# Performance work log

Measured on AMD Instinct MI355X. Metric: run time of the kernel, lower is better.

Reference implementation:

```python
import jax, jax.numpy as jnp
import numpy as np

B, N, K, DIM, NB, RES, PAD = 2, 8192, 16, 64, 5, 64, 0.1
H = DIM // 2  # bottleneck width of FKABlock
PLANES = ((0, 1), (0, 2), (1, 2))  # xy, xz, yz


def setup_inputs() -> dict:
    key = jax.random.key(0)
    ks = jax.random.split(key, 10)
    xyz = jax.random.uniform(ks[0], (B, N, 3), jnp.float32) - 0.5

    def w(k, shape, fan_in):
        return jax.random.normal(k, shape, jnp.float32) / np.sqrt(fan_in)

    return {
        "xyz": xyz,
        "w_stem": w(ks[1], (3, DIM), 3),
        "b_stem": jnp.zeros((DIM,), jnp.float32),
        "w0": w(ks[2], (NB, DIM, H), DIM),
        "b0": jnp.zeros((NB, H), jnp.float32),
        "fc1": w(ks[3], (NB, 3, K), 3),
        "fc2": w(ks[4], (NB, 2 * K, K), 2 * K),
        "fc3": w(ks[5], (NB, 2 * K, K), 2 * K),
        "wcv": w(ks[6], (NB, H, H, K), H * K),
        "alpha": jnp.ones((NB,), jnp.float32),
        "beta": jnp.ones((NB,), jnp.float32),
        "w2": w(ks[7], (NB, H, DIM), H),
        "b2": jnp.zeros((NB, DIM), jnp.float32),
    }


def _knn_idx(xyz, k):
    # brute-force squared distances (b, n, n); top-k smallest -> neighbor indices
    sq = jnp.sum(xyz * xyz, -1)
    d2 = sq[:, :, None] + sq[:, None, :] - 2.0 * jnp.einsum('bnd,bmd->bnm', xyz, xyz)
    _, idx = jax.lax.top_k(-d2, k)
    return idx  # (b, n, k) int32


_gather = jax.vmap(lambda f, i: f[i])  # (n, c), (n, k) -> (n, k, c), vmapped over batch


def _fkaconv(x, xyz, idx, fc1, fc2, fc3, wcv, alpha, beta):
    nb_pos = _gather(xyz, idx)                 # (b, n, k, 3)
    pts = nb_pos - xyz[:, :, None, :]          # local coordinates
    # distances are detached in the original (pts.detach())
    dists = jnp.sqrt(jnp.sum(jax.lax.stop_gradient(pts) ** 2, -1) + 1e-12)  # (b, n, k)
    dw = jax.nn.sigmoid(-alpha * dists + beta)
    dw = dw / (jnp.sum(dw, -1, keepdims=True) + 1e-6) * K
    dwe = dw[..., None]                        # (b, n, k, 1)
    # kernel-weight estimation MLP with masked max-pool over neighbors
    m = jax.nn.relu(pts @ fc1)                 # (b, n, k, K)
    mp = jnp.max(m * dwe, 2, keepdims=True)
    m = jax.nn.relu(jnp.concatenate([m, jnp.broadcast_to(mp, m.shape)], -1) @ fc2)
    mp = jnp.max(m * dwe, 2, keepdims=True)
    m = jax.nn.relu(jnp.concatenate([m, jnp.broadcast_to(mp, m.shape)], -1) @ fc3)
    m = m * dwe                                # (b, n, k, K)
    nb_x = _gather(x, idx)                     # (b, n, k, h)
    # f[b,n,c,s] = sum_k nb_x * m ; out[b,n,o] = sum_{c,s} f * wcv[o,c,s]
    return jnp.einsum('bnkc,bnks,ocs->bno', nb_x, m, wcv)


def _triplane(c, xyz):
    pn = xyz / (1.0 + PAD + 1e-3) + 0.5        # normalize to [0, 1]
    ij = jnp.clip((pn * RES).astype(jnp.int32), 0, RES - 1)  # (b, n, 3)
    bidx = jnp.arange(B, dtype=jnp.int32)[:, None]
    cf = c.reshape(B * N, DIM)
    ones = jnp.ones((B * N,), c.dtype)
    planes = []
    for a, b2 in PLANES:
        seg = (bidx * (RES * RES) + ij[..., a] * RES + ij[..., b2]).reshape(-1)
        s = jax.ops.segment_sum(cf, seg, num_segments=B * RES * RES)
        cnt = jax.ops.segment_sum(ones, seg, num_segments=B * RES * RES)
        planes.append((s / jnp.maximum(cnt, 1.0)[:, None]).reshape(B, RES, RES, DIM))
    return jnp.stack(planes, 1)                # (b, 3, res, res, dim)


def reference(xyz, w_stem, b_stem, w0, b0, fc1, fc2, fc3, wcv, alpha, beta, w2, b2):
    c = xyz @ w_stem + b_stem                  # stem linear
    idx = _knn_idx(xyz, K)                     # knn_points(xyz, xyz, K)
    for i in range(NB):                        # FKABlock residual blocks
        x = jax.nn.relu(c @ w0[i] + b0[i])
        x = jax.nn.relu(_fkaconv(x, xyz, idx, fc1[i], fc2[i], fc3[i], wcv[i], alpha[i], beta[i]))
        x = x @ w2[i] + b2[i]
        c = jax.nn.relu(x + c)
    tri_feat = _triplane(c, xyz)
    return (xyz, c, tri_feat)
```

## Files before the change

### kernel.cpp

```cpp
#include <hip/hip_runtime.h>
#include <math.h>

#define BB 2
#define NN 8192
#define KK 16
#define DIMM 64
#define HH 32
#define NBB 5
#define RESS 64
#define NPTS (BB*NN)
#define PLANE_ELEMS (BB*3*RESS*RESS*DIMM)
#define PLANE_CELLS (BB*3*RESS*RESS)
#define GC 8
#define GCS 0.125f
#define NCELL (GC*GC*GC)
#define CAP 2496

__global__ void zero_kernel(float* __restrict__ p, int n) {
  int t = blockIdx.x * blockDim.x + threadIdx.x;
  if (t < n) p[t] = 0.0f;
}

__global__ void stem_kernel(const float* __restrict__ xyz,
                            const float* __restrict__ w,
                            const float* __restrict__ bias,
                            float* __restrict__ out_xyz,
                            float* __restrict__ c) {
  int tid = blockIdx.x * blockDim.x + threadIdx.x;
  if (tid < NPTS*3) out_xyz[tid] = xyz[tid];
  if (tid < NPTS*DIMM) {
    int p = tid >> 6, d = tid & 63;
    float x = xyz[p*3+0], y = xyz[p*3+1], z = xyz[p*3+2];
    c[tid] = x*w[d] + y*w[64+d] + z*w[128+d] + bias[d];
  }
}

__device__ __forceinline__ unsigned ord32(float f) {
  unsigned u = __float_as_uint(f);
  return u ^ ((unsigned)((int)u >> 31) | 0x80000000u);
}
__device__ __forceinline__ int cell_of(float v) {
  return min(max((int)((v + 0.5f) * 8.0f), 0), 7);
}

__global__ void knn_count_kernel(const float* __restrict__ xyz,
                                 int* __restrict__ cellcnt) {
  int p = blockIdx.x * blockDim.x + threadIdx.x;
  if (p >= NPTS) return;
  int bq = p >> 13;
  float px = xyz[p*3], py = xyz[p*3+1], pz = xyz[p*3+2];
  int cc = (cell_of(px) << 6) | (cell_of(py) << 3) | cell_of(pz);
  atomicAdd(&cellcnt[(bq << 9) | cc], 1);
}

__global__ __launch_bounds__(1024) void knn_scan_kernel(const int* __restrict__ cnt,
                                                        int* __restrict__ cellstart,
                                                        int* __restrict__ cellcur) {
  __shared__ int s[1024];
  int t = threadIdx.x;
  int v = cnt[t];
  s[t] = v;
  __syncthreads();
  for (int off = 1; off < 1024; off <<= 1) {
    int add = (t >= off) ? s[t-off] : 0;
    __syncthreads();
    s[t] += add;
    __syncthreads();
  }
  int inc = s[t];
  cellstart[t+1] = inc;
  if (t == 0) cellstart[0] = 0;
  cellcur[t] = inc - v;
}

__global__ void knn_scatter_kernel(const float* __restrict__ xyz,
                                   int* __restrict__ cellcur,
                                   float4* __restrict__ spts) {
  int p = blockIdx.x * blockDim.x + threadIdx.x;
  if (p >= NPTS) return;
  int bq = p >> 13;
  float px = xyz[p*3], py = xyz[p*3+1], pz = xyz[p*3+2];
  int cc = (cell_of(px) << 6) | (cell_of(py) << 3) | cell_of(pz);
  int pos = atomicAdd(&cellcur[(bq << 9) | cc], 1);
  spts[pos] = make_float4(px, py, pz, __int_as_float(p & (NN-1)));
}

#define INS64(key)                                                             \
  {                                                                            \
    unsigned long long _k = (key);                                             \
    _Pragma("unroll")                                                          \
    for (int jj = 15; jj >= 1; --jj) {                                         \
      unsigned long long up = bd[jj-1];                                        \
      bool shift = _k < up;                                                    \
      bool here  = _k < bd[jj];                                                \
      unsigned long long nv = shift ? up : _k;                                 \
      bd[jj] = here ? nv : bd[jj];                                             \
    }                                                                          \
    bd[0] = (_k < bd[0]) ? _k : bd[0];                                         \
  }

#define TRYKEY(c4)                                                             \
  {                                                                            \
    float sq = (c4).x*(c4).x + (c4).y*(c4).y + (c4).z*(c4).z;                  \
    float d2 = (qs + sq) - 2.0f*(qx*(c4).x + qy*(c4).y + qz*(c4).z);           \
    unsigned du = ord32(d2);                                                   \
    bool hit = valid && du <= hi15;                                            \
    if (__any(hit)) {                                                          \
      unsigned long long key = hit ?                                           \
          (((unsigned long long)du << 32) | (unsigned)__float_as_int((c4).w))  \
          : ~0ull;                                                             \
      INS64(key);                                                              \
      hi15 = (unsigned)(bd[15] >> 32);                                         \
    }                                                                          \
  }

#define MERGE_STEP(MASK)                                                       \
  {                                                                            \
    unsigned long long tmp[16];                                                \
    _Pragma("unroll")                                                          \
    for (int j = 0; j < 16; ++j) tmp[j] = __shfl_xor(bd[j], MASK);             \
    _Pragma("unroll")                                                          \
    for (int j = 0; j < 16; ++j) {                                             \
      unsigned long long _in = tmp[j];                                         \
      bool dup = false;                                                        \
      _Pragma("unroll")                                                        \
      for (int jj = 0; jj < 16; ++jj) dup = dup || (bd[jj] == _in);            \
      INS64(dup ? ~0ull : _in);                                                \
    }                                                                          \
    hi15 = (unsigned)(bd[15] >> 32);                                           \
  }

__global__ __launch_bounds__(64) void knn_query_kernel(
    const float4* __restrict__ spts, const int* __restrict__ cellstart,
    int* __restrict__ idx) {
  __shared__ __align__(16) float4 s_cand[CAP];
  __shared__ int s_ofs[28];
  __shared__ int s_jlo[27];
  int wave = blockIdx.x;
  int b = wave >> 9;
  int cell = wave & 511;
  int cx = cell >> 6, cy = (cell >> 3) & 7, cz = cell & 7;
  int cb = b << 9;
  int qlo = cellstart[cb + cell], qhi = cellstart[cb + cell + 1];
  int nq = qhi - qlo;
  if (nq <= 0) return;
  int lane = threadIdx.x;
  int q = lane & 15, s = lane >> 4;

  int x0 = max(cx-1,0), x1 = min(cx+1,7);
  int y0 = max(cy-1,0), y1 = min(cy+1,7);
  int z0 = max(cz-1,0), z1 = min(cz+1,7);
  int dy = y1-y0+1, dz = z1-z0+1;
  int count = (x1-x0+1)*dy*dz;
  int len = 0, jlo0 = 0;
  if (lane < count) {
    int xx = x0 + lane/(dy*dz);
    int rem = lane % (dy*dz);
    int yy = y0 + rem/dz, zz = z0 + rem % dz;
    int cc = cb + (xx<<6) + (yy<<3) + zz;
    jlo0 = cellstart[cc];
    len = cellstart[cc+1] - jlo0;
  }
  int pre = len;
#pragma unroll
  for (int off = 1; off < 64; off <<= 1) {
    int v = __shfl_up(pre, off);
    if (lane >= off) pre += v;
  }
  if (lane < count) { s_ofs[lane] = pre - len; s_jlo[lane] = jlo0; }
  if (lane == count-1) s_ofs[count] = pre;
  __syncthreads();
  int total = s_ofs[count];
  int tstag = min(total, CAP);

  for (int w = lane; w < tstag; w += 64) {
    int lo2 = 0, hi2 = count-1;
    while (lo2 < hi2) { int mid = (lo2+hi2+1)>>1; if (s_ofs[mid] <= w) lo2 = mid; else hi2 = mid-1; }
    s_cand[w] = spts[s_jlo[lo2] + (w - s_ofs[lo2])];
  }
  __syncthreads();

  const unsigned thru1 = ord32((GCS - 1e-4f)*(GCS - 1e-4f));
  for (int qg = 0; qg < nq; qg += 16) {
    bool valid = (qg + q) < nq;
    float4 qv = spts[qlo + qg + (valid ? q : 0)];
    float qx = qv.x, qy = qv.y, qz = qv.z;
    float qs = qx*qx + qy*qy + qz*qz;
    unsigned long long bd[16];
#pragma unroll
    for (int j = 0; j < 16; ++j) bd[j] = ~0ull;
    unsigned hi15 = 0xFFFFFFFFu;

    int chunk = (tstag + 3) >> 2;
    int jb = s*chunk, je = min(jb+chunk, tstag);
    for (int j = jb; j < je; ++j) {
      float4 c4 = s_cand[j];
      TRYKEY(c4);
    }
    if (total > CAP) {
      for (int i = 0; i < count; ++i) {
        int ofs_i = s_ofs[i], len_i = s_ofs[i+1]-ofs_i;
        int stg = min(max(CAP - ofs_i, 0), len_i);
        int jl = s_jlo[i] + stg, jh = s_jlo[i] + len_i;
        for (int j2 = jl + s; j2 < jh; j2 += 4) {
          float4 c4 = spts[j2];
          TRYKEY(c4);
        }
      }
    }
    MERGE_STEP(16);
    MERGE_STEP(32);
    bool done = !valid || (hi15 < thru1);
    for (int r = 2; r <= 8; ++r) {
      if (!__any(!done)) break;
      int xs0 = max(cx-r,0), xs1 = min(cx+r,7);
      int ys0 = max(cy-r,0), ys1 = min(cy+r,7);
      int zs0 = max(cz-r,0), zs1 = min(cz+r,7);
      int pr = r-1;
      for (int xx = xs0; xx <= xs1; ++xx)
      for (int yy = ys0; yy <= ys1; ++yy)
      for (int zz = zs0; zz <= zs1; ++zz) {
        if (xx >= cx-pr && xx <= cx+pr && yy >= cy-pr && yy <= cy+pr &&
            zz >= cz-pr && zz <= cz+pr) continue;
        int cc2 = cb + (xx<<6) + (yy<<3) + zz;
        int jl = cellstart[cc2], jh = cellstart[cc2+1];
        for (int j2 = jl + s; j2 < jh; j2 += 4) {
          float4 c4 = spts[j2];
          TRYKEY(c4);
        }
      }
      MERGE_STEP(16);
      MERGE_STEP(32);
      float thr2 = (float)r * GCS - 1e-4f;
      done = !valid || (hi15 < ord32(thr2*thr2));
    }
    if (valid && s == 0) {
      int n_self = __float_as_int(qv.w);
      int* op = idx + (((long)b << 13) + n_self) * 16;
#pragma unroll
      for (int j = 0; j < 16; ++j) op[j] = (int)(unsigned)(bd[j] & 0xffffffffu);
    }
  }
}

__global__ void xproj_kernel(const float* __restrict__ c,
                             const float* __restrict__ w0,
                             const float* __restrict__ b0,
                             float* __restrict__ x, int layer) {
  int tid = blockIdx.x * blockDim.x + threadIdx.x;
  if (tid >= NPTS*HH) return;
  int p = tid >> 5, h = tid & 31;
  const float* w = w0 + layer*DIMM*HH;
  const float* cr = c + p*DIMM;
  float acc = b0[layer*HH + h];
#pragma unroll
  for (int d = 0; d < DIMM; ++d) acc += cr[d]*w[d*HH + h];
  x[tid] = fmaxf(acc, 0.0f);
}

#define OFF_W1   0
#define OFF_W2AT 48
#define OFF_W2BT 368
#define OFF_W3AT 688
#define OFF_W3BT 1008
#define OFF_WL   1328
#define OFF_B2   3376
#define OFF_RED  3440
#define OFF_Y    4464
#define OFF_SCR  4592
#define SCR_SZ   1296
#define S_DW 0
#define S_M1 16
#define S_M2 272
#define S_MM 528
#define S_XN 784
#define S_FB 16
#define LDS_TOT (OFF_SCR + 4*SCR_SZ)

__global__ __launch_bounds__(256) void conv_kernel(
    float* __restrict__ c, const float* __restrict__ x,
    const int* __restrict__ idx, const float* __restrict__ xyz,
    const float* __restrict__ fc1, const float* __restrict__ fc2,
    const float* __restrict__ fc3, const float* __restrict__ wcv,
    const float* __restrict__ alpha, const float* __restrict__ beta,
    const float* __restrict__ w2, const float* __restrict__ b2, int layer)
{
  __shared__ __align__(16) float lds[LDS_TOT];
  int t = threadIdx.x;

  const float* fc1l = fc1 + layer*3*KK;
  const float* fc2l = fc2 + layer*2*KK*KK;
  const float* fc3l = fc3 + layer*2*KK*KK;
  const float* wcvl = wcv + layer*HH*HH*KK;
  const float* w2l  = w2  + layer*HH*DIMM;
  const float* b2l  = b2  + layer*DIMM;

  if (t < 48) lds[OFF_W1 + t] = fc1l[t];
  {
    int s = t >> 4, tt = t & 15;
    lds[OFF_W2AT + s*20 + tt] = fc2l[tt*16 + s];
    lds[OFF_W2BT + s*20 + tt] = fc2l[(16+tt)*16 + s];
    lds[OFF_W3AT + s*20 + tt] = fc3l[tt*16 + s];
    lds[OFF_W3BT + s*20 + tt] = fc3l[(16+tt)*16 + s];
  }
#pragma unroll
  for (int r = 0; r < 8; ++r) lds[OFF_WL + t + 256*r] = w2l[t + 256*r];
  if (t < 64) lds[OFF_B2 + t] = b2l[t];
  __syncthreads();

  int wv = t >> 6, lane = t & 63;
  int p = blockIdx.x*4 + wv;
  int b = p >> 13;
  float* scr = lds + OFF_SCR + wv*SCR_SZ;
  int sI = lane & 15;

  float qxx = xyz[p*3+0], qyy = xyz[p*3+1], qzz = xyz[p*3+2];
  float alv = alpha[layer], bev = beta[layer];
  int jidx = 0; float px = 0, py = 0, pz = 0, sv = 0;
  if (lane < 16) {
    jidx = idx[p*16 + lane];
    const float* nb = xyz + ((long)b*NN + jidx)*3;
    px = nb[0]-qxx; py = nb[1]-qyy; pz = nb[2]-qzz;
    float dd = sqrtf(px*px + py*py + pz*pz + 1e-12f);
    sv = 1.0f/(1.0f + expf(alv*dd - bev));
  }
  float ssum = 0.0f;
#pragma unroll
  for (int k = 0; k < 16; ++k) ssum += __shfl(sv, k);
  if (lane < 16) scr[S_DW + lane] = sv / (ssum + 1e-6f) * 16.0f;
#pragma unroll
  for (int r = 0; r < 2; ++r) {
    int tsk = lane + 64*r;
    int k = tsk >> 3, seg = tsk & 7;
    int jk = __shfl(jidx, k);
    float4 v = *(const float4*)(x + ((long)b*NN + jk)*32 + seg*4);
    *(float4*)&scr[S_XN + k*32 + seg*4] = v;
  }
#pragma unroll
  for (int r = 0; r < 4; ++r) {
    int k = (lane >> 4) + 4*r;
    float pxk = __shfl(px, k), pyk = __shfl(py, k), pzk = __shfl(pz, k);
    float v = pxk*lds[OFF_W1+sI] + pyk*lds[OFF_W1+16+sI] + pzk*lds[OFF_W1+32+sI];
    scr[S_M1 + k*16 + sI] = fmaxf(v, 0.0f);
  }
  __syncthreads();

  {
    float mpv = 0.0f;
#pragma unroll
    for (int k = 0; k < 16; ++k) mpv = fmaxf(mpv, scr[S_M1 + k*16 + sI] * scr[S_DW + k]);
    float qv = 0.0f;
#pragma unroll
    for (int tt = 0; tt < 16; ++tt) qv += __shfl(mpv, tt) * lds[OFF_W2BT + sI*20 + tt];
    float4 wa0 = *(float4*)&lds[OFF_W2AT + sI*20 + 0];
    float4 wa1 = *(float4*)&lds[OFF_W2AT + sI*20 + 4];
    float4 wa2 = *(float4*)&lds[OFF_W2AT + sI*20 + 8];
    float4 wa3 = *(float4*)&lds[OFF_W2AT + sI*20 + 12];
#pragma unroll
    for (int r = 0; r < 4; ++r) {
      int k = (lane >> 4) + 4*r;
      float4 m0 = *(float4*)&scr[S_M1 + k*16 + 0];
      float4 m1_ = *(float4*)&scr[S_M1 + k*16 + 4];
      float4 m2_ = *(float4*)&scr[S_M1 + k*16 + 8];
      float4 m3_ = *(float4*)&scr[S_M1 + k*16 + 12];
      float v = qv;
      v += m0.x*wa0.x; v += m0.y*wa0.y; v += m0.z*wa0.z; v += m0.w*wa0.w;
      v += m1_.x*wa1.x; v += m1_.y*wa1.y; v += m1_.z*wa1.z; v += m1_.w*wa1.w;
      v += m2_.x*wa2.x; v += m2_.y*wa2.y; v += m2_.z*wa2.z; v += m2_.w*wa2.w;
      v += m3_.x*wa3.x; v += m3_.y*wa3.y; v += m3_.z*wa3.z; v += m3_.w*wa3.w;
      scr[S_M2 + k*16 + sI] = fmaxf(v, 0.0f);
    }
  }
  __syncthreads();

  {
    float mpv = 0.0f;
#pragma unroll
    for (int k = 0; k < 16; ++k) mpv = fmaxf(mpv, scr[S_M2 + k*16 + sI] * scr[S_DW + k]);
    float qv = 0.0f;
#pragma unroll
    for (int tt = 0; tt < 16; ++tt) qv += __shfl(mpv, tt) * lds[OFF_W3BT + sI*20 + tt];
    float4 wa0 = *(float4*)&lds[OFF_W3AT + sI*20 + 0];
    float4 wa1 = *(float4*)&lds[OFF_W3AT + sI*20 + 4];
    float4 wa2 = *(float4*)&lds[OFF_W3AT + sI*20 + 8];
    float4 wa3 = *(float4*)&lds[OFF_W3AT + sI*20 + 12];
#pragma unroll
    for (int r = 0; r < 4; ++r) {
      int k = (lane >> 4) + 4*r;
      float4 m0 = *(float4*)&scr[S_M2 + k*16 + 0];
      float4 m1_ = *(float4*)&scr[S_M2 + k*16 + 4];
      float4 m2_ = *(float4*)&scr[S_M2 + k*16 + 8];
      float4 m3_ = *(float4*)&scr[S_M2 + k*16 + 12];
      float v = qv;
      v += m0.x*wa0.x; v += m0.y*wa0.y; v += m0.z*wa0.z; v += m0.w*wa0.w;
      v += m1_.x*wa1.x; v += m1_.y*wa1.y; v += m1_.z*wa1.z; v += m1_.w*wa1.w;
      v += m2_.x*wa2.x; v += m2_.y*wa2.y; v += m2_.z*wa2.z; v += m2_.w*wa2.w;
      v += m3_.x*wa3.x; v += m3_.y*wa3.y; v += m3_.z*wa3.z; v += m3_.w*wa3.w;
      scr[S_MM + k*16 + sI] = fmaxf(v, 0.0f) * scr[S_DW + k];
    }
  }
  __syncthreads();

  {
    int q4 = lane >> 4;
    float fr0=0,fr1=0,fr2=0,fr3=0,fr4=0,fr5=0,fr6=0,fr7=0;
#pragma unroll
    for (int k = 0; k < 16; ++k) {
      float mmv = scr[S_MM + k*16 + sI];
      float4 a  = *(float4*)&scr[S_XN + k*32 + q4*8];
      float4 bb = *(float4*)&scr[S_XN + k*32 + q4*8 + 4];
      fr0 += a.x*mmv;  fr1 += a.y*mmv;  fr2 += a.z*mmv;  fr3 += a.w*mmv;
      fr4 += bb.x*mmv; fr5 += bb.y*mmv; fr6 += bb.z*mmv; fr7 += bb.w*mmv;
    }
    scr[S_FB + (q4*8+0)*16 + sI] = fr0;
    scr[S_FB + (q4*8+1)*16 + sI] = fr1;
    scr[S_FB + (q4*8+2)*16 + sI] = fr2;
    scr[S_FB + (q4*8+3)*16 + sI] = fr3;
    scr[S_FB + (q4*8+4)*16 + sI] = fr4;
    scr[S_FB + (q4*8+5)*16 + sI] = fr5;
    scr[S_FB + (q4*8+6)*16 + sI] = fr6;
    scr[S_FB + (q4*8+7)*16 + sI] = fr7;
  }
  __syncthreads();

  {
    int o = t & 31, seg = t >> 5;
    const float4* wrow = (const float4*)(wcvl + o*512 + seg*64);
    float acc0=0, acc1=0, acc2=0, acc3=0;
#pragma unroll
    for (int j = 0; j < 16; ++j) {
      float4 w4 = wrow[j];
      float4 f0 = *(const float4*)&lds[OFF_SCR + 0*SCR_SZ + S_FB + seg*64 + j*4];
      float4 f1 = *(const float4*)&lds[OFF_SCR + 1*SCR_SZ + S_FB + seg*64 + j*4];
      float4 f2 = *(const float4*)&lds[OFF_SCR + 2*SCR_SZ + S_FB + seg*64 + j*4];
      float4 f3 = *(const float4*)&lds[OFF_SCR + 3*SCR_SZ + S_FB + seg*64 + j*4];
      acc0 += w4.x*f0.x; acc0 += w4.y*f0.y; acc0 += w4.z*f0.z; acc0 += w4.w*f0.w;
      acc1 += w4.x*f1.x; acc1 += w4.y*f1.y; acc1 += w4.z*f1.z; acc1 += w4.w*f1.w;
      acc2 += w4.x*f2.x; acc2 += w4.y*f2.y; acc2 += w4.z*f2.z; acc2 += w4.w*f2.w;
      acc3 += w4.x*f3.x; acc3 += w4.y*f3.y; acc3 += w4.z*f3.z; acc3 += w4.w*f3.w;
    }
    lds[OFF_RED + seg*128 + 0*32 + o] = acc0;
    lds[OFF_RED + seg*128 + 1*32 + o] = acc1;
    lds[OFF_RED + seg*128 + 2*32 + o] = acc2;
    lds[OFF_RED + seg*128 + 3*32 + o] = acc3;
  }
  __syncthreads();

  if (t < 128) {
    int pt = t >> 5, o = t & 31;
    float yv = 0.0f;
#pragma unroll
    for (int seg = 0; seg < 8; ++seg) yv += lds[OFF_RED + seg*128 + pt*32 + o];
    lds[OFF_Y + pt*32 + o] = fmaxf(yv, 0.0f);
  }
  __syncthreads();

  {
    int pt = t >> 6, d = t & 63;
    float zv = lds[OFF_B2 + d];
#pragma unroll
    for (int o = 0; o < 32; ++o) zv += lds[OFF_Y + pt*32 + o] * lds[OFF_WL + o*64 + d];
    int gp = blockIdx.x*4 + pt;
    float cv = c[gp*64 + d];
    c[gp*64 + d] = fmaxf(zv + cv, 0.0f);
  }
}

__global__ void triacc_kernel(const float* __restrict__ c,
                              const float* __restrict__ xyz,
                              float* __restrict__ psum,
                              float* __restrict__ pcnt) {
  int tid = blockIdx.x * blockDim.x + threadIdx.x;
  if (tid >= NPTS*DIMM) return;
  int p = tid >> 6, d = tid & 63;
  int b = p >> 13;
  float p0 = xyz[p*3+0] / 1.101f + 0.5f;
  float p1 = xyz[p*3+1] / 1.101f + 0.5f;
  float p2 = xyz[p*3+2] / 1.101f + 0.5f;
  int i0 = min(max((int)(p0*64.0f), 0), 63);
  int i1 = min(max((int)(p1*64.0f), 0), 63);
  int i2 = min(max((int)(p2*64.0f), 0), 63);
  int cb = b*3*RESS*RESS;
  int c0 = cb + 0*RESS*RESS + i0*RESS + i1;
  int c1 = cb + 1*RESS*RESS + i0*RESS + i2;
  int c2 = cb + 2*RESS*RESS + i1*RESS + i2;
  float v = c[tid];
  atomicAdd(&psum[c0*DIMM + d], v);
  atomicAdd(&psum[c1*DIMM + d], v);
  atomicAdd(&psum[c2*DIMM + d], v);
  if (d == 0) {
    atomicAdd(&pcnt[c0], 1.0f);
    atomicAdd(&pcnt[c1], 1.0f);
    atomicAdd(&pcnt[c2], 1.0f);
  }
}

__global__ void trinorm_kernel(const float* __restrict__ psum,
                               const float* __restrict__ pcnt,
                               float* __restrict__ out) {
  int tid = blockIdx.x * blockDim.x + threadIdx.x;
  if (tid >= PLANE_ELEMS) return;
  float cnt = pcnt[tid >> 6];
  out[tid] = psum[tid] / fmaxf(cnt, 1.0f);
}

extern "C" void kernel_launch(void* const* d_in, const int* in_sizes, int n_in,
                              void* d_out, int out_size, void* d_ws, size_t ws_size,
                              hipStream_t stream) {
  const float* xyz   = (const float*)d_in[0];
  const float* wstem = (const float*)d_in[1];
  const float* bstem = (const float*)d_in[2];
  const float* w0    = (const float*)d_in[3];
  const float* b0    = (const float*)d_in[4];
  const float* fc1   = (const float*)d_in[5];
  const float* fc2   = (const float*)d_in[6];
  const float* fc3   = (const float*)d_in[7];
  const float* wcv   = (const float*)d_in[8];
  const float* alpha = (const float*)d_in[9];
  const float* beta  = (const float*)d_in[10];
  const float* w2    = (const float*)d_in[11];
  const float* b2    = (const float*)d_in[12];

  float* out     = (float*)d_out;
  float* out_xyz = out;
  float* c       = out + NPTS*3;
  float* out_tri = c + NPTS*DIMM;

  float* wsf  = (float*)d_ws;
  int*   idx  = (int*)d_ws;
  float* x    = wsf + NPTS*16;
  float* psum = x + NPTS*HH;
  float* pcnt = psum + PLANE_ELEMS;

  int*    cellcnt   = (int*)psum;
  int*    cellstart = (int*)psum + 1024;
  int*    cellcur   = (int*)psum + 2056;
  float4* spts      = (float4*)(psum + 4096);

  stem_kernel<<<(NPTS*DIMM+255)/256, 256, 0, stream>>>(xyz, wstem, bstem, out_xyz, c);
  zero_kernel<<<4, 256, 0, stream>>>((float*)cellcnt, 1024);
  knn_count_kernel<<<(NPTS+255)/256, 256, 0, stream>>>(xyz, cellcnt);
  knn_scan_kernel<<<1, 1024, 0, stream>>>(cellcnt, cellstart, cellcur);
  knn_scatter_kernel<<<(NPTS+255)/256, 256, 0, stream>>>(xyz, cellcur, spts);
  knn_query_kernel<<<1024, 64, 0, stream>>>(spts, cellstart, idx);
  for (int layer = 0; layer < NBB; ++layer) {
    xproj_kernel<<<(NPTS*HH+255)/256, 256, 0, stream>>>(c, w0, b0, x, layer);
    conv_kernel<<<NPTS/4, 256, 0, stream>>>(c, x, idx, xyz, fc1, fc2, fc3, wcv,
                                            alpha, beta, w2, b2, layer);
  }
  int nz = PLANE_ELEMS + PLANE_CELLS;
  zero_kernel<<<(nz+255)/256, 256, 0, stream>>>(psum, nz);
  triacc_kernel<<<(NPTS*DIMM+255)/256, 256, 0, stream>>>(c, xyz, psum, pcnt);
  trinorm_kernel<<<(PLANE_ELEMS+255)/256, 256, 0, stream>>>(psum, pcnt, out_tri);
}
```

Before: 586.4 us.

## Split kNN query per cell across two blocks and merge partial top-k

The kNN query for each grid cell now runs in two workgroups instead of one. Each takes alternating neighbour cells and writes its own 64-bit top-16 distance/index keys to a workspace buffer. A new merge kernel combines the two lists into the final neighbour indices. The aim is to double block-level parallelism in a launch of 1024 single-wave blocks that underfills the GPU. The cost is an extra kernel launch and global traffic for the partial lists, and each half may expand to more search rings because it sees fewer candidates.

```diff
diff --git a/kernel.cpp b/kernel.cpp
--- a/kernel.cpp
+++ b/kernel.cpp
@@ -14,7 +14,7 @@
 #define GC 8
 #define GCS 0.125f
 #define NCELL (GC*GC*GC)
-#define CAP 2496
+#define CAP 768
 
 __global__ void zero_kernel(float* __restrict__ p, int n) {
   int t = blockIdx.x * blockDim.x + threadIdx.x;
@@ -130,13 +130,14 @@
     hi15 = (unsigned)(bd[15] >> 32);                                           \
   }
 
-__global__ __launch_bounds__(64) void knn_query_kernel(
+__global__ __launch_bounds__(64) void knn_part_kernel(
     const float4* __restrict__ spts, const int* __restrict__ cellstart,
-    int* __restrict__ idx) {
+    unsigned long long* __restrict__ part) {
   __shared__ __align__(16) float4 s_cand[CAP];
-  __shared__ int s_ofs[28];
-  __shared__ int s_jlo[27];
-  int wave = blockIdx.x;
+  __shared__ int s_ofs[16];
+  __shared__ int s_jlo[15];
+  int wave = blockIdx.x >> 1;
+  int h = blockIdx.x & 1;
   int b = wave >> 9;
   int cell = wave & 511;
   int cx = cell >> 6, cy = (cell >> 3) & 7, cz = cell & 7;
@@ -152,10 +153,12 @@
   int z0 = max(cz-1,0), z1 = min(cz+1,7);
   int dy = y1-y0+1, dz = z1-z0+1;
   int count = (x1-x0+1)*dy*dz;
+  int mycount = (count - h + 1) >> 1;
   int len = 0, jlo0 = 0;
-  if (lane < count) {
-    int xx = x0 + lane/(dy*dz);
-    int rem = lane % (dy*dz);
+  int i = 2*lane + h;
+  if (lane < mycount) {
+    int xx = x0 + i/(dy*dz);
+    int rem = i % (dy*dz);
     int yy = y0 + rem/dz, zz = z0 + rem % dz;
     int cc = cb + (xx<<6) + (yy<<3) + zz;
     jlo0 = cellstart[cc];
@@ -167,14 +170,14 @@
     int v = __shfl_up(pre, off);
     if (lane >= off) pre += v;
   }
-  if (lane < count) { s_ofs[lane] = pre - len; s_jlo[lane] = jlo0; }
-  if (lane == count-1) s_ofs[count] = pre;
-  __syncthreads();
-  int total = s_ofs[count];
+  if (lane < mycount) { s_ofs[lane] = pre - len; s_jlo[lane] = jlo0; }
+  if (lane == mycount-1) s_ofs[mycount] = pre;
+  __syncthreads();
+  int total = s_ofs[mycount];
   int tstag = min(total, CAP);
 
   for (int w = lane; w < tstag; w += 64) {
-    int lo2 = 0, hi2 = count-1;
+    int lo2 = 0, hi2 = mycount-1;
     while (lo2 < hi2) { int mid = (lo2+hi2+1)>>1; if (s_ofs[mid] <= w) lo2 = mid; else hi2 = mid-1; }
     s_cand[w] = spts[s_jlo[lo2] + (w - s_ofs[lo2])];
   }
@@ -198,10 +201,10 @@
       TRYKEY(c4);
     }
     if (total > CAP) {
-      for (int i = 0; i < count; ++i) {
-        int ofs_i = s_ofs[i], len_i = s_ofs[i+1]-ofs_i;
+      for (int ii = 0; ii < mycount; ++ii) {
+        int ofs_i = s_ofs[ii], len_i = s_ofs[ii+1]-ofs_i;
         int stg = min(max(CAP - ofs_i, 0), len_i);
-        int jl = s_jlo[i] + stg, jh = s_jlo[i] + len_i;
+        int jl = s_jlo[ii] + stg, jh = s_jlo[ii] + len_i;
         for (int j2 = jl + s; j2 < jh; j2 += 4) {
           float4 c4 = spts[j2];
           TRYKEY(c4);
@@ -217,11 +220,14 @@
       int ys0 = max(cy-r,0), ys1 = min(cy+r,7);
       int zs0 = max(cz-r,0), zs1 = min(cz+r,7);
       int pr = r-1;
+      int ri = 0;
       for (int xx = xs0; xx <= xs1; ++xx)
       for (int yy = ys0; yy <= ys1; ++yy)
       for (int zz = zs0; zz <= zs1; ++zz) {
         if (xx >= cx-pr && xx <= cx+pr && yy >= cy-pr && yy <= cy+pr &&
             zz >= cz-pr && zz <= cz+pr) continue;
+        int take = ((ri & 1) == h); ri++;
+        if (!take) continue;
         int cc2 = cb + (xx<<6) + (yy<<3) + zz;
         int jl = cellstart[cc2], jh = cellstart[cc2+1];
         for (int j2 = jl + s; j2 < jh; j2 += 4) {
@@ -235,12 +241,29 @@
       done = !valid || (hi15 < ord32(thr2*thr2));
     }
     if (valid && s == 0) {
-      int n_self = __float_as_int(qv.w);
-      int* op = idx + (((long)b << 13) + n_self) * 16;
-#pragma unroll
-      for (int j = 0; j < 16; ++j) op[j] = (int)(unsigned)(bd[j] & 0xffffffffu);
-    }
-  }
+      int qpos = qlo + qg + q;
+      unsigned long long* op = part + (long)qpos*32 + h*16;
+#pragma unroll
+      for (int j = 0; j < 16; ++j) op[j] = bd[j];
+    }
+  }
+}
+
+__global__ void knn_merge_kernel(const float4* __restrict__ spts,
+                                 const unsigned long long* __restrict__ part,
+                                 int* __restrict__ idx) {
+  int qpos = blockIdx.x * blockDim.x + threadIdx.x;
+  if (qpos >= NPTS) return;
+  unsigned long long bd[16];
+#pragma unroll
+  for (int j = 0; j < 16; ++j) bd[j] = part[(long)qpos*32 + j];
+#pragma unroll
+  for (int j = 0; j < 16; ++j) { INS64(part[(long)qpos*32 + 16 + j]); }
+  int b = qpos >> 13;
+  int n_self = __float_as_int(spts[qpos].w);
+  int* op = idx + (((long)b << 13) + n_self) * 16;
+#pragma unroll
+  for (int j = 0; j < 16; ++j) op[j] = (int)(unsigned)(bd[j] & 0xffffffffu);
 }
 
 __global__ void xproj_kernel(const float* __restrict__ c,
@@ -536,13 +559,15 @@
   int*    cellstart = (int*)psum + 1024;
   int*    cellcur   = (int*)psum + 2056;
   float4* spts      = (float4*)(psum + 4096);
+  unsigned long long* part = (unsigned long long*)(psum + 69632);
 
   stem_kernel<<<(NPTS*DIMM+255)/256, 256, 0, stream>>>(xyz, wstem, bstem, out_xyz, c);
   zero_kernel<<<4, 256, 0, stream>>>((float*)cellcnt, 1024);
   knn_count_kernel<<<(NPTS+255)/256, 256, 0, stream>>>(xyz, cellcnt);
   knn_scan_kernel<<<1, 1024, 0, stream>>>(cellcnt, cellstart, cellcur);
   knn_scatter_kernel<<<(NPTS+255)/256, 256, 0, stream>>>(xyz, cellcur, spts);
-  knn_query_kernel<<<1024, 64, 0, stream>>>(spts, cellstart, idx);
+  knn_part_kernel<<<2048, 64, 0, stream>>>(spts, cellstart, part);
+  knn_merge_kernel<<<(NPTS+255)/256, 256, 0, stream>>>(spts, part, idx);
   for (int layer = 0; layer < NBB; ++layer) {
     xproj_kernel<<<(NPTS*HH+255)/256, 256, 0, stream>>>(c, w0, b0, x, layer);
     conv_kernel<<<NPTS/4, 256, 0, stream>>>(c, x, idx, xyz, fc1, fc2, fc3, wcv,
```

Result: slower. 631.7 us (+7.7%).
